# Kernel optimization log

Hardware: AMD Instinct MI355X
Metric: run time of the kernel (lower is better)

The kernel has to match this reference:

```python
import jax, jax.numpy as jnp
import numpy as np

B, N, E, D, H = 32, 2048, 1024, 1024, 1024


def setup_inputs() -> dict:
    key = jax.random.key(0)
    k_enc, k_dec, k_we, k_wd, k_wo = jax.random.split(key, 5)
    enc = jax.random.normal(k_enc, (B, N, E), dtype=jnp.float32)
    dec = jax.random.normal(k_dec, (B, D), dtype=jnp.float32)
    inp_mask = jnp.ones((B, N), dtype=bool)
    # params initialized like torch.rand -> uniform [0,1)
    w_e = jax.random.uniform(k_we, (E, H), dtype=jnp.float32)
    w_d = jax.random.uniform(k_wd, (D, H), dtype=jnp.float32)
    w_out = jax.random.uniform(k_wo, (H, 1), dtype=jnp.float32)
    return {"enc": enc, "dec": dec, "inp_mask": inp_mask,
            "w_e": w_e, "w_d": w_d, "w_out": w_out}


def reference(enc, dec, inp_mask, w_e, w_d, w_out):
    # hidden: [B, N, H]
    h = jnp.tanh(enc @ w_e + (dec @ w_d)[:, None, :])
    scores = (h @ w_out)[..., 0]                      # [B, N]
    scores = jnp.where(inp_mask, scores, -jnp.inf)    # mask invalid positions
    probs = jax.nn.softmax(scores, axis=-1)           # [B, N]
    attn = jnp.einsum('bn,bne->be', probs, enc)       # weighted sum of enc
    return attn, probs
```

## Files before the change

### kernel.cpp

```cpp
#include <hip/hip_runtime.h>
#include <hip/hip_bf16.h>

typedef _Float16 half8 __attribute__((ext_vector_type(8)));
typedef float f32x4 __attribute__((ext_vector_type(4)));

#define Bsz 32
#define Nseq 2048
#define Edim 1024
#define Hdim 1024

__device__ __forceinline__ void gload_lds16(const void* g, void* l) {
    __builtin_amdgcn_global_load_lds(
        (const __attribute__((address_space(1))) unsigned int*)g,
        (__attribute__((address_space(3))) unsigned int*)l, 16, 0, 0);
}

__global__ void k_dw(const float* __restrict__ dec, const float* __restrict__ w_d,
                     float* __restrict__ dw) {
    int b = blockIdx.x;
    int h = blockIdx.y * 256 + threadIdx.x;
    const float* dr = dec + b * 1024;
    float a0 = 0.f, a1 = 0.f, a2 = 0.f, a3 = 0.f;
    for (int d = 0; d < 1024; d += 4) {
        a0 += dr[d + 0] * w_d[(d + 0) * 1024 + h];
        a1 += dr[d + 1] * w_d[(d + 1) * 1024 + h];
        a2 += dr[d + 2] * w_d[(d + 2) * 1024 + h];
        a3 += dr[d + 3] * w_d[(d + 3) * 1024 + h];
    }
    dw[b * 1024 + h] = (a0 + a1) + (a2 + a3);
}

__global__ void k_split(const float* __restrict__ w_e,
                        _Float16* __restrict__ w_hiT, _Float16* __restrict__ w_loT) {
    __shared__ _Float16 th[32][33];
    __shared__ _Float16 tl[32][33];
    int e0 = blockIdx.x * 32, h0 = blockIdx.y * 32;
    int tx = threadIdx.x & 31, ty = threadIdx.x >> 5;
#pragma unroll
    for (int i = 0; i < 4; ++i) {
        int r = ty + i * 8;
        float x = w_e[(size_t)(e0 + r) * 1024 + h0 + tx];
        _Float16 h = (_Float16)x;
        th[r][tx] = h;
        tl[r][tx] = (_Float16)(x - (float)h);
    }
    __syncthreads();
#pragma unroll
    for (int i = 0; i < 4; ++i) {
        int r = ty + i * 8;
        w_hiT[(size_t)(h0 + r) * 1024 + e0 + tx] = th[tx][r];
        w_loT[(size_t)(h0 + r) * 1024 + e0 + tx] = tl[tx][r];
    }
}

__global__ __launch_bounds__(512, 4)
void k_scores(const float* __restrict__ enc,
              const _Float16* __restrict__ w_hiT, const _Float16* __restrict__ w_loT,
              const float* __restrict__ dw, const float* __restrict__ w_out,
              float* __restrict__ scores) {
    extern __shared__ __align__(16) char smem[];
    float* scoreL = (float*)(smem + 65536);

    const int tid  = threadIdx.x;
    const int lane = tid & 63;
    const int wave = tid >> 6;
    const int wr = wave >> 2, wc = wave & 3;
    const int m0 = blockIdx.x * 128;
    const int bb = m0 >> 11;
    const float* dwb = dw + bb * 1024;
    const int rb = lane & 15, ksl = lane >> 4;

    const int a_row = tid >> 2, a_ks = tid & 3;
    const float* aBase = enc + (size_t)(m0 + a_row) * 1024 + a_ks * 8;
    const int aWofs = (a_row >> 1) * 128 + (a_row & 1) * 64
                    + ((a_ks ^ ((a_row >> 1) & 3)) << 4);
    const int bRow0 = 2 * (tid >> 3) + ((tid >> 2) & 1);
    const int bD    = ((tid & 3) ^ ((tid >> 3) & 3)) << 4;
    const char* whiB = (const char*)w_hiT;
    const char* wloB = (const char*)w_loT;

    const int p2 = rb >> 1;
    const int swz = (ksl ^ (p2 & 3)) << 4;
    const int aRd = wr * 4096 + p2 * 128 + (rb & 1) * 64 + swz;
    const int bRd = wc * 2048 + p2 * 128 + (rb & 1) * 64 + swz;

    if (tid < 128) scoreL[tid] = 0.f;

    f32x4 acc[4][2];
#pragma unroll
    for (int m = 0; m < 4; ++m)
#pragma unroll
        for (int n = 0; n < 2; ++n) acc[m][n] = (f32x4){0.f, 0.f, 0.f, 0.f};

    float4 pa0, pa1;

#define A_LOAD(t) do { \
        const float* _p = aBase + (((t) & 31) << 5); \
        pa0 = ((const float4*)_p)[0]; \
        pa1 = ((const float4*)_p)[1]; \
    } while (0)
#define B_ISSUE(t, buf) do { \
        const size_t _g = ((size_t)((t) >> 5) << 18) + (size_t)((t) & 31) * 64 \
                        + (size_t)bRow0 * 2048 + bD; \
        char* _b = smem + 32768 + (buf) * 16384; \
        gload_lds16(whiB + _g, _b + tid * 16); \
        gload_lds16(wloB + _g, _b + 8192 + tid * 16); \
    } while (0)
#define A_STAGE(buf) do { \
        float _q[8] = {pa0.x, pa0.y, pa0.z, pa0.w, pa1.x, pa1.y, pa1.z, pa1.w}; \
        half8 _hi, _lo; \
        _Pragma("unroll") \
        for (int _j = 0; _j < 8; ++_j) { \
            _Float16 _h = (_Float16)_q[_j]; \
            _hi[_j] = _h; \
            _lo[_j] = (_Float16)(_q[_j] - (float)_h); \
        } \
        char* _a = smem + (buf) * 16384; \
        *(half8*)(_a + aWofs)        = _hi; \
        *(half8*)(_a + 8192 + aWofs) = _lo; \
    } while (0)

    A_LOAD(0);
    B_ISSUE(0, 0);
    A_STAGE(0);
    A_LOAD(1);
    __syncthreads();

    for (int t = 0; t < 256; ++t) {
        const int cur = t & 1;
        if (t < 255) {
            B_ISSUE(t + 1, cur ^ 1);
            A_STAGE(cur ^ 1);
            if (t < 254) A_LOAD(t + 2);
        }
        const char* sa = smem + cur * 16384;
        const char* sb = smem + 32768 + cur * 16384;

        half8 bh[2], bl[2];
#pragma unroll
        for (int n = 0; n < 2; ++n) {
            bh[n] = *(const half8*)(sb + bRd + n * 1024);
            bl[n] = *(const half8*)(sb + 8192 + bRd + n * 1024);
        }
        __builtin_amdgcn_s_setprio(1);
#pragma unroll
        for (int m = 0; m < 4; ++m) {
            half8 ah = *(const half8*)(sa + aRd + m * 1024);
            half8 al = *(const half8*)(sa + 8192 + aRd + m * 1024);
#pragma unroll
            for (int n = 0; n < 2; ++n) {
                acc[m][n] = __builtin_amdgcn_mfma_f32_16x16x32_f16(ah, bh[n], acc[m][n], 0, 0, 0);
                acc[m][n] = __builtin_amdgcn_mfma_f32_16x16x32_f16(ah, bl[n], acc[m][n], 0, 0, 0);
                acc[m][n] = __builtin_amdgcn_mfma_f32_16x16x32_f16(al, bh[n], acc[m][n], 0, 0, 0);
            }
        }
        __builtin_amdgcn_s_setprio(0);

        if ((t & 31) == 31) {
            const int hc = t >> 5;
#pragma unroll
            for (int m = 0; m < 4; ++m) {
                float con[4] = {0.f, 0.f, 0.f, 0.f};
#pragma unroll
                for (int n = 0; n < 2; ++n) {
                    int h = hc * 128 + wc * 32 + n * 16 + rb;
                    float dwv = dwb[h];
                    float wo  = w_out[h];
#pragma unroll
                    for (int r = 0; r < 4; ++r) {
                        float x = acc[m][n][r] + dwv;
                        float e = __expf(2.0f * fabsf(x));
                        float th = copysignf(1.0f - __fdividef(2.0f, e + 1.0f), x);
                        con[r] += th * wo;
                    }
                    acc[m][n] = (f32x4){0.f, 0.f, 0.f, 0.f};
                }
#pragma unroll
                for (int r = 0; r < 4; ++r) {
                    float v = con[r];
                    v += __shfl_xor(v, 1);
                    v += __shfl_xor(v, 2);
                    v += __shfl_xor(v, 4);
                    v += __shfl_xor(v, 8);
                    con[r] = v;
                }
                if (rb == 0) {
                    int rbase = wr * 64 + m * 16 + ksl * 4;
#pragma unroll
                    for (int r = 0; r < 4; ++r)
                        atomicAdd(&scoreL[rbase + r], con[r]);
                }
            }
        }
        __syncthreads();
    }

    __syncthreads();
    if (tid < 128) scores[m0 + tid] = scoreL[tid];
#undef A_LOAD
#undef B_ISSUE
#undef A_STAGE
}

__global__ void k_softmax(const float* __restrict__ scores,
                          const int* __restrict__ mask,
                          float* __restrict__ probs, float* __restrict__ out_probs) {
    int b = blockIdx.x, tid = threadIdx.x;
    __shared__ float red[8];
    float v[8];
    float m = -INFINITY;
#pragma unroll
    for (int i = 0; i < 8; ++i) {
        int n = tid + i * 256;
        float s = scores[b * 2048 + n];
        s = (mask[b * 2048 + n] != 0) ? s : -INFINITY;
        v[i] = s;
        m = fmaxf(m, s);
    }
    for (int off = 32; off; off >>= 1) m = fmaxf(m, __shfl_xor(m, off));
    if ((tid & 63) == 0) red[tid >> 6] = m;
    __syncthreads();
    m = fmaxf(fmaxf(red[0], red[1]), fmaxf(red[2], red[3]));
    float sum = 0.f;
#pragma unroll
    for (int i = 0; i < 8; ++i) {
        v[i] = expf(v[i] - m);
        sum += v[i];
    }
    for (int off = 32; off; off >>= 1) sum += __shfl_xor(sum, off);
    if ((tid & 63) == 0) red[4 + (tid >> 6)] = sum;
    __syncthreads();
    sum = red[4] + red[5] + red[6] + red[7];
    float inv = 1.0f / sum;
#pragma unroll
    for (int i = 0; i < 8; ++i) {
        int n = tid + i * 256;
        float p = v[i] * inv;
        probs[b * 2048 + n]     = p;
        out_probs[b * 2048 + n] = p;
    }
}

__global__ void k_attn(const float* __restrict__ probs, const float* __restrict__ enc,
                       float* __restrict__ attn) {
    __shared__ float pv[128];
    __shared__ int   pidx[128];
    __shared__ int   cnt;
    int b = blockIdx.x, c = blockIdx.y, t = threadIdx.x;
    if (t == 0) cnt = 0;
    __syncthreads();
    if (t < 128) {
        float p = probs[b * 2048 + c * 128 + t];
        if (p >= 1e-12f) {
            int slot = atomicAdd(&cnt, 1);
            pv[slot]   = p;
            pidx[slot] = c * 128 + t;
        }
    }
    __syncthreads();
    int nk = cnt;
    if (nk == 0) return;
    const float* eb = enc + (size_t)b * 2048 * 1024;
    float4 acc = {0.f, 0.f, 0.f, 0.f};
    for (int i = 0; i < nk; ++i) {
        float p = pv[i];
        float4 v = ((const float4*)(eb + (size_t)pidx[i] * 1024))[t];
        acc.x += p * v.x;
        acc.y += p * v.y;
        acc.z += p * v.z;
        acc.w += p * v.w;
    }
    float* o = attn + b * 1024 + t * 4;
    atomicAdd(o + 0, acc.x);
    atomicAdd(o + 1, acc.y);
    atomicAdd(o + 2, acc.z);
    atomicAdd(o + 3, acc.w);
}

extern "C" void kernel_launch(void* const* d_in, const int* in_sizes, int n_in,
                              void* d_out, int out_size, void* d_ws, size_t ws_size,
                              hipStream_t stream) {
    const float* enc   = (const float*)d_in[0];
    const float* dec   = (const float*)d_in[1];
    const int*   mask  = (const int*)d_in[2];
    const float* w_e   = (const float*)d_in[3];
    const float* w_d   = (const float*)d_in[4];
    const float* w_out = (const float*)d_in[5];

    float* out_attn  = (float*)d_out;
    float* out_probs = out_attn + Bsz * Hdim;

    float* dw        = (float*)d_ws;
    float* scores    = dw + Bsz * Hdim;
    float* probs     = scores + Bsz * Nseq;
    _Float16* w_hiT  = (_Float16*)(probs + Bsz * Nseq);
    _Float16* w_loT  = w_hiT + Edim * Hdim;

    static const int kScoresLds = 66048;
    hipFuncSetAttribute((const void*)k_scores,
                        hipFuncAttributeMaxDynamicSharedMemorySize, kScoresLds);

    hipMemsetAsync(out_attn, 0, Bsz * Hdim * sizeof(float), stream);
    k_dw<<<dim3(32, 4), dim3(256), 0, stream>>>(dec, w_d, dw);
    k_split<<<dim3(32, 32), dim3(256), 0, stream>>>(w_e, w_hiT, w_loT);
    k_scores<<<dim3(512), dim3(512), kScoresLds, stream>>>(enc, w_hiT, w_loT, dw, w_out, scores);
    k_softmax<<<dim3(32), dim3(256), 0, stream>>>(scores, mask, probs, out_probs);
    k_attn<<<dim3(32, 16), dim3(256), 0, stream>>>(probs, enc, out_attn);
}
```

Before: 467.4 us.

## Split main GEMM loop into two phases interleaving loads with MFMA clusters

```diff
diff --git a/kernel.cpp b/kernel.cpp
--- a/kernel.cpp
+++ b/kernel.cpp
@@ -119,41 +119,76 @@
         *(half8*)(_a + aWofs)        = _hi; \
         *(half8*)(_a + 8192 + aWofs) = _lo; \
     } while (0)
+#define MFMA_PAIR(ma) do { \
+        _Pragma("unroll") \
+        for (int n = 0; n < 2; ++n) \
+            acc[(ma)][n]   = __builtin_amdgcn_mfma_f32_16x16x32_f16(ah0, bh[n], acc[(ma)][n], 0, 0, 0); \
+        _Pragma("unroll") \
+        for (int n = 0; n < 2; ++n) \
+            acc[(ma)+1][n] = __builtin_amdgcn_mfma_f32_16x16x32_f16(ah1, bh[n], acc[(ma)+1][n], 0, 0, 0); \
+        _Pragma("unroll") \
+        for (int n = 0; n < 2; ++n) \
+            acc[(ma)][n]   = __builtin_amdgcn_mfma_f32_16x16x32_f16(ah0, bl[n], acc[(ma)][n], 0, 0, 0); \
+        _Pragma("unroll") \
+        for (int n = 0; n < 2; ++n) \
+            acc[(ma)+1][n] = __builtin_amdgcn_mfma_f32_16x16x32_f16(ah1, bl[n], acc[(ma)+1][n], 0, 0, 0); \
+        _Pragma("unroll") \
+        for (int n = 0; n < 2; ++n) \
+            acc[(ma)][n]   = __builtin_amdgcn_mfma_f32_16x16x32_f16(al0, bh[n], acc[(ma)][n], 0, 0, 0); \
+        _Pragma("unroll") \
+        for (int n = 0; n < 2; ++n) \
+            acc[(ma)+1][n] = __builtin_amdgcn_mfma_f32_16x16x32_f16(al1, bh[n], acc[(ma)+1][n], 0, 0, 0); \
+    } while (0)
+#define LOAD_A_FRAG2(m) do { \
+        ah0 = *(const half8*)(sa + aRd + (m) * 1024); \
+        al0 = *(const half8*)(sa + 8192 + aRd + (m) * 1024); \
+        ah1 = *(const half8*)(sa + aRd + ((m) + 1) * 1024); \
+        al1 = *(const half8*)(sa + 8192 + aRd + ((m) + 1) * 1024); \
+    } while (0)
 
     A_LOAD(0);
     B_ISSUE(0, 0);
     A_STAGE(0);
     A_LOAD(1);
-    __syncthreads();
+    B_ISSUE(1, 1);
+    asm volatile("s_waitcnt vmcnt(4) lgkmcnt(0)" ::: "memory");
+    __builtin_amdgcn_sched_barrier(0);
+    __builtin_amdgcn_s_barrier();
 
     for (int t = 0; t < 256; ++t) {
         const int cur = t & 1;
-        if (t < 255) {
-            B_ISSUE(t + 1, cur ^ 1);
-            A_STAGE(cur ^ 1);
-            if (t < 254) A_LOAD(t + 2);
-        }
         const char* sa = smem + cur * 16384;
         const char* sb = smem + 32768 + cur * 16384;
-
         half8 bh[2], bl[2];
+        half8 ah0, al0, ah1, al1;
+
+        LOAD_A_FRAG2(0);
 #pragma unroll
         for (int n = 0; n < 2; ++n) {
             bh[n] = *(const half8*)(sb + bRd + n * 1024);
             bl[n] = *(const half8*)(sb + 8192 + bRd + n * 1024);
         }
+        if (t < 255) B_ISSUE(t + 1, cur ^ 1);
+        __builtin_amdgcn_s_barrier();
+        asm volatile("s_waitcnt lgkmcnt(0)" ::: "memory");
+        __builtin_amdgcn_sched_barrier(0);
         __builtin_amdgcn_s_setprio(1);
-#pragma unroll
-        for (int m = 0; m < 4; ++m) {
-            half8 ah = *(const half8*)(sa + aRd + m * 1024);
-            half8 al = *(const half8*)(sa + 8192 + aRd + m * 1024);
-#pragma unroll
-            for (int n = 0; n < 2; ++n) {
-                acc[m][n] = __builtin_amdgcn_mfma_f32_16x16x32_f16(ah, bh[n], acc[m][n], 0, 0, 0);
-                acc[m][n] = __builtin_amdgcn_mfma_f32_16x16x32_f16(ah, bl[n], acc[m][n], 0, 0, 0);
-                acc[m][n] = __builtin_amdgcn_mfma_f32_16x16x32_f16(al, bh[n], acc[m][n], 0, 0, 0);
-            }
+        MFMA_PAIR(0);
+        __builtin_amdgcn_s_setprio(0);
+        __builtin_amdgcn_s_barrier();
+
+        LOAD_A_FRAG2(2);
+        if (t < 255) A_STAGE(cur ^ 1);
+        if (t < 254) A_LOAD(t + 2);
+        __builtin_amdgcn_s_barrier();
+        if (t < 254) {
+            asm volatile("s_waitcnt vmcnt(2) lgkmcnt(0)" ::: "memory");
+        } else {
+            asm volatile("s_waitcnt vmcnt(0) lgkmcnt(0)" ::: "memory");
         }
+        __builtin_amdgcn_sched_barrier(0);
+        __builtin_amdgcn_s_setprio(1);
+        MFMA_PAIR(2);
         __builtin_amdgcn_s_setprio(0);
 
         if ((t & 31) == 31) {
@@ -192,7 +227,7 @@
                 }
             }
         }
-        __syncthreads();
+        __builtin_amdgcn_s_barrier();
     }
 
     __syncthreads();
@@ -200,6 +235,8 @@
 #undef A_LOAD
 #undef B_ISSUE
 #undef A_STAGE
+#undef MFMA_PAIR
+#undef LOAD_A_FRAG2
 }
 
 __global__ void k_softmax(const float* __restrict__ scores,
```

Measured after the change: 482.7 us. 3.3% more time.
